# Kernel optimization log

Measured on AMD Instinct MI355X. Metric: run time of the kernel, lower is better.

Reference implementation:

```python
import jax, jax.numpy as jnp
import numpy as np

N_NODES = 100000
D_FEAT = 128
B = 50000
NUM_SAMPLE = 10


def setup_inputs() -> dict:
    key = jax.random.key(0)
    k1, k2, k3, k4 = jax.random.split(key, 4)
    nodes = jax.random.randint(k1, (B,), 0, N_NODES, dtype=jnp.int64 if jax.config.jax_enable_x64 else jnp.int32)
    neighbor_idx = jax.random.randint(k2, (B, NUM_SAMPLE), 0, N_NODES)
    neighbor_count = jax.random.randint(k3, (B,), 0, NUM_SAMPLE + 1)
    features = jax.random.normal(k4, (N_NODES, D_FEAT), dtype=jnp.float32)
    return {"nodes": nodes, "neighbor_idx": neighbor_idx,
            "neighbor_count": neighbor_count, "features": features}


def reference(nodes, neighbor_idx, neighbor_count, features):
    # Gather sampled neighbor features: [B, S, d]
    neigh_feats = features[neighbor_idx]
    S = neighbor_idx.shape[1]
    # Mask out padding slots beyond each node's sampled neighbor count.
    mask = (jnp.arange(S)[None, :] < neighbor_count[:, None]).astype(features.dtype)  # [B, S]
    summed = jnp.einsum('bsd,bs->bd', neigh_feats, mask)
    denom = jnp.maximum(neighbor_count, 1).astype(features.dtype)[:, None]
    mean_feats = summed / denom
    # Empty neighbor list -> fall back to the node's own feature (unsqueeze+mean == identity).
    own_feats = features[nodes]
    return jnp.where((neighbor_count == 0)[:, None], own_feats, mean_feats)
```

## Files before the change

### kernel.cpp

```cpp
#include <hip/hip_runtime.h>
#include <hip/hip_bf16.h>


#define B_NODES 50000
#define NUM_SAMPLE 10
#define D_FEAT 128
#define VEC_PER_ROW (D_FEAT / 4)

__global__ __launch_bounds__(256) void mean_agg_kernel(
    const int* __restrict__ nodes,
    const int* __restrict__ neighbor_idx,
    const int* __restrict__ neighbor_count,
    const float4* __restrict__ features4,
    float4* __restrict__ out4)
{
    const int node = blockIdx.x * 8 + (threadIdx.x >> 5);
    const int lane = threadIdx.x & 31;
    if (node >= B_NODES) return;

    const int cnt = neighbor_count[node];
    const int own = nodes[node];

    const int2* nb2 = (const int2*)(neighbor_idx + node * NUM_SAMPLE);
    const int2 q0 = nb2[0], q1 = nb2[1], q2 = nb2[2], q3 = nb2[3], q4 = nb2[4];
    const int idx[NUM_SAMPLE] = {q0.x, q0.y, q1.x, q1.y, q2.x, q2.y, q3.x, q3.y, q4.x, q4.y};

    float4 v[NUM_SAMPLE];
    #pragma unroll
    for (int s = 0; s < NUM_SAMPLE; ++s) {
        v[s] = make_float4(0.f, 0.f, 0.f, 0.f);
        if (s < cnt) v[s] = features4[idx[s] * VEC_PER_ROW + lane];
    }

    float4 acc = make_float4(0.f, 0.f, 0.f, 0.f);
    if (cnt == 0) acc = features4[own * VEC_PER_ROW + lane];

    #pragma unroll
    for (int s = 0; s < NUM_SAMPLE; ++s) {
        acc.x += v[s].x;
        acc.y += v[s].y;
        acc.z += v[s].z;
        acc.w += v[s].w;
    }

    const float inv = 1.0f / (float)((cnt > 1) ? cnt : 1);
    acc.x *= inv; acc.y *= inv; acc.z *= inv; acc.w *= inv;
    out4[node * VEC_PER_ROW + lane] = acc;
}

extern "C" void kernel_launch(void* const* d_in, const int* in_sizes, int n_in,
                              void* d_out, int out_size, void* d_ws, size_t ws_size,
                              hipStream_t stream) {
    const int*    nodes          = (const int*)d_in[0];
    const int*    neighbor_idx   = (const int*)d_in[1];
    const int*    neighbor_count = (const int*)d_in[2];
    const float4* features4      = (const float4*)d_in[3];
    float4*       out4           = (float4*)d_out;

    const int nodes_per_block = 8;
    const int grid = (B_NODES + nodes_per_block - 1) / nodes_per_block;
    mean_agg_kernel<<<grid, 256, 0, stream>>>(nodes, neighbor_idx, neighbor_count,
                                              features4, out4);
}
```

Baseline: 28.83 us.

## Process two nodes per thread with branch-free gathers and nontemporal stores

Each 32-lane group now aggregates two nodes, doubling the loads in flight per thread and halving the grid. Gathers for inactive sample slots are redirected to an already-loaded row, so all 20 loads issue unconditionally and padding is handled with 0/1 weights in the accumulation. Outputs use nontemporal stores to avoid polluting cache. The redundant loads add some L2/TLB traffic, and more registers per thread may lower occupancy.

```diff
diff --git a/kernel.cpp b/kernel.cpp
--- a/kernel.cpp
+++ b/kernel.cpp
@@ -6,59 +6,78 @@
 #define NUM_SAMPLE 10
 #define D_FEAT 128
 #define VEC_PER_ROW (D_FEAT / 4)
+#define NODES_PER_BLOCK 16
+
+typedef float f32x4 __attribute__((ext_vector_type(4)));
 
 __global__ __launch_bounds__(256) void mean_agg_kernel(
     const int* __restrict__ nodes,
     const int* __restrict__ neighbor_idx,
     const int* __restrict__ neighbor_count,
-    const float4* __restrict__ features4,
-    float4* __restrict__ out4)
+    const f32x4* __restrict__ features4,
+    f32x4* __restrict__ out4)
 {
-    const int node = blockIdx.x * 8 + (threadIdx.x >> 5);
+    const int grp  = threadIdx.x >> 5;
     const int lane = threadIdx.x & 31;
-    if (node >= B_NODES) return;
+    const int nA = blockIdx.x * NODES_PER_BLOCK + grp;
+    const int nB = nA + 8;
 
-    const int cnt = neighbor_count[node];
-    const int own = nodes[node];
+    const int cntA = neighbor_count[nA];
+    const int cntB = neighbor_count[nB];
+    const int ownA = nodes[nA];
+    const int ownB = nodes[nB];
 
-    const int2* nb2 = (const int2*)(neighbor_idx + node * NUM_SAMPLE);
-    const int2 q0 = nb2[0], q1 = nb2[1], q2 = nb2[2], q3 = nb2[3], q4 = nb2[4];
-    const int idx[NUM_SAMPLE] = {q0.x, q0.y, q1.x, q1.y, q2.x, q2.y, q3.x, q3.y, q4.x, q4.y};
+    const int2* a2 = (const int2*)(neighbor_idx + nA * NUM_SAMPLE);
+    const int2* b2 = (const int2*)(neighbor_idx + nB * NUM_SAMPLE);
+    const int2 a0 = a2[0], a1 = a2[1], a2_ = a2[2], a3 = a2[3], a4 = a2[4];
+    const int2 b0 = b2[0], b1 = b2[1], b2_ = b2[2], b3 = b2[3], b4 = b2[4];
+    const int idxA[NUM_SAMPLE] = {a0.x, a0.y, a1.x, a1.y, a2_.x, a2_.y, a3.x, a3.y, a4.x, a4.y};
+    const int idxB[NUM_SAMPLE] = {b0.x, b0.y, b1.x, b1.y, b2_.x, b2_.y, b3.x, b3.y, b4.x, b4.y};
 
-    float4 v[NUM_SAMPLE];
+    const int baseA = (cntA == 0) ? ownA : idxA[0];
+    const int baseB = (cntB == 0) ? ownB : idxB[0];
+
+    f32x4 vA[NUM_SAMPLE], vB[NUM_SAMPLE];
     #pragma unroll
     for (int s = 0; s < NUM_SAMPLE; ++s) {
-        v[s] = make_float4(0.f, 0.f, 0.f, 0.f);
-        if (s < cnt) v[s] = features4[idx[s] * VEC_PER_ROW + lane];
+        const int eA = (s < cntA) ? idxA[s] : baseA;
+        vA[s] = features4[eA * VEC_PER_ROW + lane];
+    }
+    #pragma unroll
+    for (int s = 0; s < NUM_SAMPLE; ++s) {
+        const int eB = (s < cntB) ? idxB[s] : baseB;
+        vB[s] = features4[eB * VEC_PER_ROW + lane];
     }
 
-    float4 acc = make_float4(0.f, 0.f, 0.f, 0.f);
-    if (cnt == 0) acc = features4[own * VEC_PER_ROW + lane];
+    f32x4 accA = vA[0];
+    #pragma unroll
+    for (int s = 1; s < NUM_SAMPLE; ++s) {
+        const float w = (s < cntA) ? 1.0f : 0.0f;
+        accA += w * vA[s];
+    }
+    accA *= 1.0f / (float)((cntA > 1) ? cntA : 1);
+    __builtin_nontemporal_store(accA, &out4[nA * VEC_PER_ROW + lane]);
 
+    f32x4 accB = vB[0];
     #pragma unroll
-    for (int s = 0; s < NUM_SAMPLE; ++s) {
-        acc.x += v[s].x;
-        acc.y += v[s].y;
-        acc.z += v[s].z;
-        acc.w += v[s].w;
+    for (int s = 1; s < NUM_SAMPLE; ++s) {
+        const float w = (s < cntB) ? 1.0f : 0.0f;
+        accB += w * vB[s];
     }
-
-    const float inv = 1.0f / (float)((cnt > 1) ? cnt : 1);
-    acc.x *= inv; acc.y *= inv; acc.z *= inv; acc.w *= inv;
-    out4[node * VEC_PER_ROW + lane] = acc;
+    accB *= 1.0f / (float)((cntB > 1) ? cntB : 1);
+    __builtin_nontemporal_store(accB, &out4[nB * VEC_PER_ROW + lane]);
 }
 
 extern "C" void kernel_launch(void* const* d_in, const int* in_sizes, int n_in,
                               void* d_out, int out_size, void* d_ws, size_t ws_size,
                               hipStream_t stream) {
-    const int*    nodes          = (const int*)d_in[0];
-    const int*    neighbor_idx   = (const int*)d_in[1];
-    const int*    neighbor_count = (const int*)d_in[2];
-    const float4* features4      = (const float4*)d_in[3];
-    float4*       out4           = (float4*)d_out;
+    const int*   nodes          = (const int*)d_in[0];
+    const int*   neighbor_idx   = (const int*)d_in[1];
+    const int*   neighbor_count = (const int*)d_in[2];
+    const f32x4* features4      = (const f32x4*)d_in[3];
+    f32x4*       out4           = (f32x4*)d_out;
 
-    const int nodes_per_block = 8;
-    const int grid = (B_NODES + nodes_per_block - 1) / nodes_per_block;
+    const int grid = (B_NODES + NODES_PER_BLOCK - 1) / NODES_PER_BLOCK;
     mean_agg_kernel<<<grid, 256, 0, stream>>>(nodes, neighbor_idx, neighbor_count,
                                               features4, out4);
 }
```

Result: faster. 26.76 us, median of 2 (-7.2%).
